# Performance work log

Measured on AMD Instinct MI355X. Metric: run time of the kernel, lower is better.

The kernel has to match this reference:

```python
import jax, jax.numpy as jnp
import numpy as np
from jax import lax

EPS = 1e-5
GROUPS = 16

def _conv(x, w, b):
    # x: [N,C,H,W], w: [O,I,3,3]
    y = lax.conv_general_dilated(x, w, (1, 1), 'SAME',
                                 dimension_numbers=('NCHW', 'OIHW', 'NCHW'))
    return y + b[None, :, None, None]

def _group_norm(x, gamma, beta):
    N, C, H, W = x.shape
    xr = x.reshape(N, GROUPS, C // GROUPS, H, W)
    m = xr.mean(axis=(2, 3, 4), keepdims=True)
    v = xr.var(axis=(2, 3, 4), keepdims=True)
    xn = ((xr - m) * lax.rsqrt(v + EPS)).reshape(N, C, H, W)
    return xn * gamma[None, :, None, None] + beta[None, :, None, None]

def _tower(x, ws, bs, gs, betas):
    for w, b, g, bt in zip(ws, bs, gs, betas):
        x = jax.nn.relu(_group_norm(_conv(x, w, b), g, bt))
    return x

def _fcos_heads(feats, cls_w, cls_b, cls_g, cls_bt, cls_ow, cls_ob,
                reg_w, reg_b, reg_g, reg_bt, reg_ow, reg_ob, ctr_w, ctr_b):
    outs = []
    for f in feats:
        N = f.shape[0]
        c = _tower(f, cls_w, cls_b, cls_g, cls_bt)
        logits = _conv(c, cls_ow, cls_ob)                 # [N, num_classes, H, W]
        r = _tower(f, reg_w, reg_b, reg_g, reg_bt)
        bbox = jax.nn.relu(_conv(r, reg_ow, reg_ob))      # [N, 4, H, W]
        ctr = _conv(r, ctr_w, ctr_b)                      # [N, 1, H, W]
        lvl = jnp.concatenate([logits, bbox, ctr], axis=1)  # [N, num_classes+5, H, W]
        outs.append(lvl.reshape(N, lvl.shape[1], -1))
    return jnp.concatenate(outs, axis=-1)  # [N, num_classes+5, sum(H*W)]

def setup_inputs() -> dict:
    key = jax.random.key(0)
    C, NUM_CLASSES, NB = 256, 80, 2
    sizes = [(128, 128), (64, 64), (32, 32), (16, 16), (8, 8)]
    keys = iter(jax.random.split(key, 64))
    d = {}
    for i, (h, w) in enumerate(sizes):
        d[f'feat{i}'] = jax.random.normal(next(keys), (NB, C, h, w), jnp.float32)
    for head in ('cls', 'reg'):
        for i in range(3):
            d[f'{head}_w{i}'] = 0.01 * jax.random.normal(next(keys), (C, C, 3, 3), jnp.float32)
            d[f'{head}_b{i}'] = jnp.zeros((C,), jnp.float32)
            d[f'{head}_gn_g{i}'] = jnp.ones((C,), jnp.float32)
            d[f'{head}_gn_b{i}'] = jnp.zeros((C,), jnp.float32)
    d['cls_out_w'] = 0.01 * jax.random.normal(next(keys), (NUM_CLASSES, C, 3, 3), jnp.float32)
    prior = 0.01
    d['cls_out_b'] = jnp.full((NUM_CLASSES,), float(-np.log((1 - prior) / prior)), jnp.float32)
    d['reg_out_w'] = 0.01 * jax.random.normal(next(keys), (4, C, 3, 3), jnp.float32)
    d['reg_out_b'] = jnp.zeros((4,), jnp.float32)
    d['ctr_w'] = 0.01 * jax.random.normal(next(keys), (1, C, 3, 3), jnp.float32)
    d['ctr_b'] = jnp.zeros((1,), jnp.float32)
    return d

def reference(feat0, feat1, feat2, feat3, feat4,
              cls_w0, cls_b0, cls_gn_g0, cls_gn_b0,
              cls_w1, cls_b1, cls_gn_g1, cls_gn_b1,
              cls_w2, cls_b2, cls_gn_g2, cls_gn_b2,
              reg_w0, reg_b0, reg_gn_g0, reg_gn_b0,
              reg_w1, reg_b1, reg_gn_g1, reg_gn_b1,
              reg_w2, reg_b2, reg_gn_g2, reg_gn_b2,
              cls_out_w, cls_out_b, reg_out_w, reg_out_b, ctr_w, ctr_b):
    feats = [feat0, feat1, feat2, feat3, feat4]
    return _fcos_heads(feats,
                       [cls_w0, cls_w1, cls_w2], [cls_b0, cls_b1, cls_b2],
                       [cls_gn_g0, cls_gn_g1, cls_gn_g2], [cls_gn_b0, cls_gn_b1, cls_gn_b2],
                       cls_out_w, cls_out_b,
                       [reg_w0, reg_w1, reg_w2], [reg_b0, reg_b1, reg_b2],
                       [reg_gn_g0, reg_gn_g1, reg_gn_g2], [reg_gn_b0, reg_gn_b1, reg_gn_b2],
                       reg_out_w, reg_out_b, ctr_w, ctr_b)
```

## Files before the change

kernel.cpp:

```cpp
#include <hip/hip_runtime.h>
#include <stdint.h>


typedef __attribute__((ext_vector_type(8))) short short8;
typedef __attribute__((ext_vector_type(4))) float floatx4;

#define XP 349184
#define TIB (32 * XP)

__device__ __forceinline__ unsigned short f2bf(float f) {
  unsigned u = __float_as_uint(f);
  u = (u + 0x7FFFu + ((u >> 16) & 1u)) >> 16;
  return (unsigned short)u;
}
__device__ __forceinline__ unsigned pk2(float a, float b) {
  return (unsigned)f2bf(a) | ((unsigned)f2bf(b) << 16);
}
__device__ __forceinline__ void async16(const void* g, void* l) {
  __builtin_amdgcn_global_load_lds(
      (const __attribute__((address_space(1))) unsigned int*)g,
      (__attribute__((address_space(3))) unsigned int*)l, 16, 0, 0);
}

#define WAIT_VM4 0x0F74
#define WAIT_VM0 0x0F70

__device__ const int d_lw[5]   = {7, 6, 5, 4, 3};
__device__ const int d_off[5]  = {0, 16384, 20480, 21504, 21760};
__device__ const int d_nt[5]   = {128, 32, 8, 2, 1};
__device__ const int d_cumT[6] = {0, 1024, 1280, 1344, 1360, 1368};
__device__ const int d_cumO[6] = {0, 512, 640, 672, 680, 684};
__device__ const int d_cumS[6] = {0, 256, 320, 336, 340, 341};
__device__ const int ck_lvl[13] = {0,0,0,0,0,0,0,0,1,1,2,3,4};
__device__ const int ck_c0[13]  = {0,2048,4096,6144,8192,10240,12288,14336,0,2048,0,0,0};
__device__ const int ck_len[13] = {2048,2048,2048,2048,2048,2048,2048,2048,2048,2048,1024,256,64};

__global__ void zpk(float* zp, float* stats) {
  for (int i = threadIdx.x; i < 384; i += 256) zp[i] = 0.f;
  for (int i = threadIdx.x; i < 1920; i += 256) stats[i] = 0.f;
}

__global__ __launch_bounds__(256) void wtrans(
    const float* __restrict__ c0, const float* __restrict__ c1, const float* __restrict__ c2,
    const float* __restrict__ r0, const float* __restrict__ r1, const float* __restrict__ r2,
    const float* __restrict__ cw, const float* __restrict__ rw, const float* __restrict__ tw,
    unsigned short* __restrict__ dst) {
  const int z = blockIdx.y;
  const int nel = (z < 6) ? 589824 : 294912;
  const int idx = blockIdx.x * 256 + threadIdx.x;
  if (idx >= nel) return;
  int tmp = idx;
  const int j = tmp & 7;   tmp >>= 3;
  const int m = tmp & 127; tmp >>= 7;
  const int cs = tmp & 3;  tmp >>= 2;
  const int t = tmp % 9;   tmp /= 9;
  const int cc = tmp & 7;  const int mt = tmp >> 3;
  const int o = mt * 128 + m;
  const int i = cc * 32 + cs * 8 + j;
  float v = 0.f;
  const float* srcs[6] = {c0, c1, c2, r0, r1, r2};
  if (z < 6)      v = srcs[z][((size_t)o * 256 + i) * 9 + t];
  else if (z == 6){ if (o < 80) v = cw[((size_t)o * 256 + i) * 9 + t]; }
  else            { if (o < 4)  v = rw[((size_t)o * 256 + i) * 9 + t];
                    else if (o == 4) v = tw[(size_t)i * 9 + t]; }
  const size_t base = (z < 6) ? (size_t)z * 589824
                              : (size_t)6 * 589824 + (size_t)(z - 6) * 294912;
  dst[base + idx] = f2bf(v);
}

__global__ __launch_bounds__(256) void feat_nhwc(
    const float* __restrict__ s0, const float* __restrict__ s1,
    const float* __restrict__ s2, const float* __restrict__ s3,
    const float* __restrict__ s4, unsigned short* __restrict__ dst) {
  __shared__ unsigned short tile[64][65];
  int bx = blockIdx.x, lvl = 0;
  while (bx >= d_cumS[lvl + 1]) ++lvl;
  const int HW = 1 << (2 * d_lw[lvl]), off = d_off[lvl];
  const float* srcs[5] = {s0, s1, s2, s3, s4};
  const float* src = srcs[lvl];
  const int img = blockIdx.z, c0 = blockIdx.y * 64, p0 = (bx - d_cumS[lvl]) * 64;
  const float* s = src + ((size_t)img * 256 + c0) * HW + p0;
  const int tid = threadIdx.x;
#pragma unroll
  for (int i = 0; i < 4; i++) {
    const int cl = (tid >> 4) + i * 16, pl = (tid & 15) * 4;
    const float4 v = *(const float4*)(s + (size_t)cl * HW + pl);
    tile[cl][pl]     = f2bf(v.x);
    tile[cl][pl + 1] = f2bf(v.y);
    tile[cl][pl + 2] = f2bf(v.z);
    tile[cl][pl + 3] = f2bf(v.w);
  }
  __syncthreads();
  const int pl = tid >> 2, cseg = (tid & 3) * 16;
  unsigned ro[8];
#pragma unroll
  for (int k = 0; k < 8; k++)
    ro[k] = (unsigned)tile[cseg + 2 * k][pl] | ((unsigned)tile[cseg + 2 * k + 1][pl] << 16);
  const int ch0 = c0 + cseg;
  char* db = (char*)dst + (size_t)img * TIB + (size_t)(ch0 >> 3) * XP
           + (size_t)(off + p0 + pl) * 16;
  uint4 u0 = {ro[0], ro[1], ro[2], ro[3]};
  uint4 u1 = {ro[4], ro[5], ro[6], ro[7]};
  *(uint4*)db = u0;
  *(uint4*)(db + XP) = u1;
}

__global__ __launch_bounds__(256) void conv_mfma(
    const unsigned short* __restrict__ xin0, const unsigned short* __restrict__ xin1,
    const unsigned short* __restrict__ wA, const unsigned short* __restrict__ wB,
    unsigned short* __restrict__ y0, unsigned short* __restrict__ y1,
    const float* __restrict__ cb0, const float* __restrict__ cb1,
    float* __restrict__ out,
    const float* __restrict__ ob_cls, const float* __restrict__ ob_reg, const float* __restrict__ ob_ctr,
    const unsigned short* __restrict__ zp, int mode) {
  __shared__ __align__(16) char smem[49152];
  const int tid = threadIdx.x;
  const int* cum = (mode == 0) ? d_cumT : d_cumO;
  const int nwg = (mode == 0) ? 1368 : 684;
  const int xcd = blockIdx.x & 7, cidx = blockIdx.x >> 3;
  const int qq = nwg >> 3, rr = nwg & 7;
  int bid = (xcd < rr ? xcd * (qq + 1) : rr * (qq + 1) + (xcd - rr) * qq) + cidx;
  int lvl = 0;
  while (bid >= cum[lvl + 1]) ++lvl;
  int r = bid - cum[lvl];
  const int lw = d_lw[lvl], W = 1 << lw, HW = 1 << (2 * lw), poffl = d_off[lvl];
  const int ntc = d_nt[lvl];
  const int nt = r % ntc; r /= ntc;
  int mt = 0;
  if (mode == 0) { mt = r & 1; r >>= 1; }
  const int img = r & 1, tower = r >> 1;

  const unsigned short* xin = (tower ? xin1 : xin0) + (size_t)img * 21824 * 256;
  const unsigned short* wset = tower ? wB : wA;

  const int n = tid & 127;
  const int p = nt * 128 + n;
  const bool pv = p < HW;
  const int h = p >> lw, w = p & (W - 1);
  const int kq = tid >> 7;

  const char* xb = (const char*)xin;
  const char* tb[9];
  int stp[9];
#pragma unroll
  for (int t = 0; t < 9; t++) {
    const int rr2 = h + t / 3 - 1, cx = w + t % 3 - 1;
    const bool v = pv && rr2 >= 0 && rr2 < W && cx >= 0 && cx < W;
    tb[t] = v ? xb + (size_t)kq * XP + (size_t)(poffl + rr2 * W + cx) * 16
              : (const char*)zp;
    stp[t] = v ? 4 * XP : 0;
  }

  const char* abase = (const char*)wset + (size_t)mt * 589824;
  const char* a_tid = abase + (size_t)tid * 16;
  char* l_tid = smem + tid * 16;

  const int lane = tid & 63, q = lane >> 4, lr = lane & 15;
  const int wv = tid >> 6, wm = wv >> 1, wn = wv & 1;
  int aoff[4], boff[4];
#pragma unroll
  for (int i = 0; i < 4; i++) {
    aoff[i] = ((q << 7) + wm * 64 + i * 16 + lr) << 4;
    boff[i] = (((q << 7) + wn * 64 + i * 16 + lr) << 4) + 8192;
  }

  floatx4 acc[4][4];
#pragma unroll
  for (int i = 0; i < 4; i++)
#pragma unroll
    for (int j = 0; j < 4; j++) acc[i][j] = (floatx4){0.f, 0.f, 0.f, 0.f};

#define UNIT(CC, U, WIMM)                                                     \
  {                                                                           \
    const int it_ = (CC) * 9 + (U);                                           \
    __builtin_amdgcn_s_waitcnt(WIMM);                                         \
    __builtin_amdgcn_s_barrier();                                             \
    asm volatile("" ::: "memory");                                            \
    if (it_ + 2 < 72) {                                                       \
      const int nu_ = (U) + 2;                                                \
      const int tn_ = nu_ % 9;                              \
      const int ccn_ = (CC) + nu_ / 9;                                        \
      char* la_ = l_tid + (nu_ % 3) * 16384;                                  \
      const char* ap_ = a_tid + (size_t)(it_ + 2) * 8192;                     \
      async16(ap_, la_);                                                      \
      async16(ap_ + 4096, la_ + 4096);                                        \
      const int sp_ = stp[tn_];                                               \
      const char* bp_ = tb[tn_] + ccn_ * sp_;                                 \
      async16(bp_, la_ + 8192);                                               \
      async16(bp_ + (sp_ >> 1), la_ + 12288);                                 \
    }                                                                         \
    asm volatile("" ::: "memory");                                            \
    const int sb_ = ((U) % 3) * 16384;                                        \
    short8 af[4], bfr[4];                                                     \
    _Pragma("unroll")                                                         \
    for (int i = 0; i < 4; i++) {                                             \
      af[i] = *(const short8*)(smem + sb_ + aoff[i]);                         \
      bfr[i] = *(const short8*)(smem + sb_ + boff[i]);                        \
    }                                                                         \
    _Pragma("unroll")                                                         \
    for (int i = 0; i < 4; i++)                                               \
      _Pragma("unroll")                                                       \
      for (int j = 0; j < 4; j++)                                             \
        acc[i][j] = __builtin_amdgcn_mfma_f32_16x16x32_bf16(af[i], bfr[j],    \
                                                            acc[i][j], 0, 0, 0); \
  }

  async16(a_tid, l_tid);
  async16(a_tid + 4096, l_tid + 4096);
  async16(tb[0], l_tid + 8192);
  async16(tb[0] + (stp[0] >> 1), l_tid + 12288);
  async16(a_tid + 8192, l_tid + 16384);
  async16(a_tid + 12288, l_tid + 20480);
  async16(tb[1], l_tid + 24576);
  async16(tb[1] + (stp[1] >> 1), l_tid + 28672);

  for (int cc = 0; cc < 7; ++cc) {
#pragma unroll
    for (int u = 0; u < 9; ++u) UNIT(cc, u, WAIT_VM4)
  }
  UNIT(7, 0, WAIT_VM4) UNIT(7, 1, WAIT_VM4) UNIT(7, 2, WAIT_VM4)
  UNIT(7, 3, WAIT_VM4) UNIT(7, 4, WAIT_VM4) UNIT(7, 5, WAIT_VM4)
  UNIT(7, 6, WAIT_VM4) UNIT(7, 7, WAIT_VM0) UNIT(7, 8, WAIT_VM0)
#undef UNIT

  if (mode == 0) {
    char* yb = (char*)(tower ? y1 : y0) + (size_t)img * TIB;
    const float* cb = tower ? cb1 : cb0;
#pragma unroll
    for (int i = 0; i < 4; i++) {
      const int c = mt * 128 + wm * 64 + i * 16 + (q << 2);
      const float4 b4 = *(const float4*)(cb + c);
      char* yp = yb + (size_t)(c >> 3) * XP + (size_t)poffl * 16 + ((c & 7) << 1);
#pragma unroll
      for (int j = 0; j < 4; j++) {
        const int pp = nt * 128 + wn * 64 + j * 16 + lr;
        if (pp >= HW) continue;
        floatx4 a = acc[i][j];
        uint2 u;
        u.x = pk2(a.x + b4.x, a.y + b4.y);
        u.y = pk2(a.z + b4.z, a.w + b4.w);
        *(uint2*)(yp + (size_t)pp * 16) = u;
      }
    }
  } else {
#pragma unroll
    for (int j = 0; j < 4; j++) {
      const int pp = nt * 128 + wn * 64 + j * 16 + lr;
      if (pp >= HW) continue;
      const size_t gp = (size_t)poffl + pp;
#pragma unroll
      for (int i = 0; i < 4; i++) {
        const int m0 = wm * 64 + i * 16 + (q << 2);
        floatx4 a = acc[i][j];
#pragma unroll
        for (int k2 = 0; k2 < 4; k2++) {
          const int m = m0 + k2;
          const float v = a[k2];
          if (tower == 0) {
            if (m < 80) out[((size_t)img * 85 + m) * 21824 + gp] = v + ob_cls[m];
          } else {
            if (m < 4)
              out[((size_t)img * 85 + 80 + m) * 21824 + gp] = fmaxf(v + ob_reg[m], 0.f);
            else if (m == 4)
              out[((size_t)img * 85 + 84) * 21824 + gp] = v + ob_ctr[0];
          }
        }
      }
    }
  }
}

__global__ __launch_bounds__(256) void gn_stats(
    const unsigned short* __restrict__ y0, const unsigned short* __restrict__ y1,
    float* __restrict__ stats) {
  const int ck = blockIdx.x, g = blockIdx.y, tz = blockIdx.z;
  const int tower = tz >> 1, img = tz & 1;
  const int lvl = ck_lvl[ck], c0 = ck_c0[ck], len = ck_len[ck];
  const char* base = (const char*)(tower ? y1 : y0) + (size_t)img * TIB
                   + (size_t)(2 * g) * XP + (size_t)(d_off[lvl] + c0) * 16;
  const int tid = threadIdx.x;
  float s = 0.f, s2 = 0.f;
  const int n2 = 2 * len;
  for (int i = tid; i < n2; i += 256) {
    const int pl = (i >= len);
    const int pos = i - pl * len;
    const uint4 d = *(const uint4*)(base + (size_t)pl * XP + (size_t)pos * 16);
    unsigned uu[4] = {d.x, d.y, d.z, d.w};
#pragma unroll
    for (int k = 0; k < 4; k++) {
      const float f0 = __uint_as_float(uu[k] << 16);
      const float f1 = __uint_as_float(uu[k] & 0xFFFF0000u);
      s += f0 + f1;
      s2 += f0 * f0 + f1 * f1;
    }
  }
#pragma unroll
  for (int m = 1; m < 64; m <<= 1) {
    s += __shfl_xor(s, m);
    s2 += __shfl_xor(s2, m);
  }
  __shared__ float rs[4], rq[4];
  const int lane = tid & 63, wvv = tid >> 6;
  if (lane == 0) { rs[wvv] = s; rq[wvv] = s2; }
  __syncthreads();
  if (tid == 0) {
    float* st = stats + (((tz * 5 + lvl) * 16 + g) << 1);
    atomicAdd(st, rs[0] + rs[1] + rs[2] + rs[3]);
    atomicAdd(st + 1, rq[0] + rq[1] + rq[2] + rq[3]);
  }
}

__global__ __launch_bounds__(256) void gn_apply(
    const unsigned short* __restrict__ ybase, unsigned short* __restrict__ xbase,
    const float* __restrict__ stats,
    const float* __restrict__ g0, const float* __restrict__ b0,
    const float* __restrict__ g1, const float* __restrict__ b1) {
  const int g = blockIdx.x * 256 + threadIdx.x;
  const int pos = g % 21824;
  const int rest = g / 21824;
  const int plane = rest & 31;
  const int ti = rest >> 5;
  const int tower = ti >> 1;
  const int lvl = (pos >= 16384) + (pos >= 20480) + (pos >= 21504) + (pos >= 21760);
  const float cnt = (float)(16 << (2 * d_lw[lvl]));
  const float* st = stats + ((((ti * 5 + lvl) * 16 + (plane >> 1))) << 1);
  const float mean = st[0] / cnt;
  const float var = st[1] / cnt - mean * mean;
  const float rstd = rsqrtf(var + 1e-5f);
  const float* gam = (tower ? g1 : g0) + plane * 8;
  const float* bet = (tower ? b1 : b0) + plane * 8;
  const size_t off = (size_t)ti * TIB + (size_t)plane * XP + (size_t)pos * 16;
  const uint4 d = *(const uint4*)((const char*)ybase + off);
  unsigned uu[4] = {d.x, d.y, d.z, d.w};
  unsigned ro[4];
#pragma unroll
  for (int k = 0; k < 4; k++) {
    const float f0 = __uint_as_float(uu[k] << 16);
    const float f1 = __uint_as_float(uu[k] & 0xFFFF0000u);
    const float o0 = fmaxf((f0 - mean) * rstd * gam[2 * k] + bet[2 * k], 0.f);
    const float o1 = fmaxf((f1 - mean) * rstd * gam[2 * k + 1] + bet[2 * k + 1], 0.f);
    ro[k] = (unsigned)f2bf(o0) | ((unsigned)f2bf(o1) << 16);
  }
  uint4 od = {ro[0], ro[1], ro[2], ro[3]};
  *(uint4*)((char*)xbase + off) = od;
}

extern "C" void kernel_launch(void* const* d_in, const int* in_sizes, int n_in,
                              void* d_out, int out_size, void* d_ws, size_t ws_size,
                              hipStream_t stream) {
  (void)in_sizes; (void)n_in; (void)out_size; (void)ws_size;
  char* ws = (char*)d_ws;
  unsigned short* zp = (unsigned short*)ws;
  unsigned short* wblk = (unsigned short*)(ws + 2048);
  const size_t WSET_T = 1179648;
  const size_t WSET_O = 589824;
  char* pXfeat = ws + 2048 + 6 * WSET_T + 2 * WSET_O;
  const size_t XSZ = (size_t)2 * 21824 * 256 * 2;
  char* pX = pXfeat + XSZ;
  char* pY = pX + 2 * XSZ;
  float* stats = (float*)(pY + 2 * XSZ);

  zpk<<<1, 256, 0, stream>>>((float*)zp, stats);
  wtrans<<<dim3(2304, 8), 256, 0, stream>>>(
      (const float*)d_in[5], (const float*)d_in[9], (const float*)d_in[13],
      (const float*)d_in[17], (const float*)d_in[21], (const float*)d_in[25],
      (const float*)d_in[29], (const float*)d_in[31], (const float*)d_in[33], wblk);
  feat_nhwc<<<dim3(341, 4, 2), 256, 0, stream>>>(
      (const float*)d_in[0], (const float*)d_in[1], (const float*)d_in[2],
      (const float*)d_in[3], (const float*)d_in[4], (unsigned short*)pXfeat);

  unsigned short* xc = (unsigned short*)pX;
  unsigned short* xr = (unsigned short*)(pX + XSZ);
  unsigned short* yc = (unsigned short*)pY;
  unsigned short* yr = (unsigned short*)(pY + XSZ);

  for (int s = 0; s < 3; s++) {
    const unsigned short* in0 = s ? xc : (unsigned short*)pXfeat;
    const unsigned short* in1 = s ? xr : (unsigned short*)pXfeat;
    const unsigned short* wc = wblk + (size_t)s * 589824;
    const unsigned short* wr = wblk + (size_t)(3 + s) * 589824;
    float* st_s = stats + (size_t)s * 640;
    conv_mfma<<<1368, 256, 0, stream>>>(
        in0, in1, wc, wr, yc, yr,
        (const float*)d_in[6 + 4 * s], (const float*)d_in[18 + 4 * s],
        nullptr, nullptr, nullptr, nullptr, zp, 0);
    gn_stats<<<dim3(13, 16, 4), 256, 0, stream>>>(yc, yr, st_s);
    gn_apply<<<10912, 256, 0, stream>>>(
        (const unsigned short*)pY, (unsigned short*)pX, st_s,
        (const float*)d_in[7 + 4 * s], (const float*)d_in[8 + 4 * s],
        (const float*)d_in[19 + 4 * s], (const float*)d_in[20 + 4 * s]);
  }
  const unsigned short* wo_c = wblk + (size_t)6 * 589824;
  const unsigned short* wo_r = wo_c + 294912;
  conv_mfma<<<684, 256, 0, stream>>>(
      xc, xr, wo_c, wo_r, nullptr, nullptr, nullptr, nullptr,
      (float*)d_out, (const float*)d_in[30], (const float*)d_in[32],
      (const float*)d_in[34], zp, 1);
}
```

Before: 600.6 us.

## Add 128x256 tile conv kernel with triple-buffered async LDS pipeline for tower convs

Adds a new tower-conv kernel in which each block computes a 128-channel by 256-pixel tile, with every wave accumulating 4x8 MFMA fragments. Operands stream through a three-stage async global-to-LDS ring buffer, prefetching two steps ahead. Blocks are remapped across XCDs and the grid drops from 1368 to 688 blocks. The larger tile cuts redundant weight and activation loads per output, at the cost of 72KB LDS per block, heavy register use, fewer blocks, and wasted work on the small pyramid levels.

```diff
diff --git a/kernel.cpp b/kernel.cpp
--- a/kernel.cpp
+++ b/kernel.cpp
@@ -23,6 +23,7 @@
 }
 
 #define WAIT_VM4 0x0F74
+#define WAIT_VM6 0x0F76
 #define WAIT_VM0 0x0F70
 
 __device__ const int d_lw[5]   = {7, 6, 5, 4, 3};
@@ -31,6 +32,8 @@
 __device__ const int d_cumT[6] = {0, 1024, 1280, 1344, 1360, 1368};
 __device__ const int d_cumO[6] = {0, 512, 640, 672, 680, 684};
 __device__ const int d_cumS[6] = {0, 256, 320, 336, 340, 341};
+__device__ const int d_nt2[5]  = {64, 16, 4, 1, 1};
+__device__ const int d_cum2[6] = {0, 512, 640, 672, 680, 688};
 __device__ const int ck_lvl[13] = {0,0,0,0,0,0,0,0,1,1,2,3,4};
 __device__ const int ck_c0[13]  = {0,2048,4096,6144,8192,10240,12288,14336,0,2048,0,0,0};
 __device__ const int ck_len[13] = {2048,2048,2048,2048,2048,2048,2048,2048,2048,2048,1024,256,64};
@@ -270,6 +273,140 @@
   }
 }
 
+__global__ __launch_bounds__(256, 2) void conv_t256(
+    const unsigned short* __restrict__ xin0, const unsigned short* __restrict__ xin1,
+    const unsigned short* __restrict__ wA, const unsigned short* __restrict__ wB,
+    unsigned short* __restrict__ y0, unsigned short* __restrict__ y1,
+    const float* __restrict__ cb0, const float* __restrict__ cb1,
+    const unsigned short* __restrict__ zp) {
+  extern __shared__ __align__(16) char smem[];
+  const int tid = threadIdx.x;
+  const int xcd = blockIdx.x & 7, cidx = blockIdx.x >> 3;
+  int bid = xcd * 86 + cidx;
+  int lvl = 0;
+  while (bid >= d_cum2[lvl + 1]) ++lvl;
+  int r = bid - d_cum2[lvl];
+  const int lw = d_lw[lvl], W = 1 << lw, HW = 1 << (2 * lw), poffl = d_off[lvl];
+  const int ntc = d_nt2[lvl];
+  const int nt = r % ntc; r /= ntc;
+  const int mt = r & 1; r >>= 1;
+  const int img = r & 1, tower = r >> 1;
+
+  const char* xb = (const char*)((tower ? xin1 : xin0)) + (size_t)img * TIB;
+  const unsigned short* wset = tower ? wB : wA;
+
+  const int p = nt * 256 + tid;
+  const bool pv = p < HW;
+  const int h = p >> lw, w = p & (W - 1);
+
+  const char* tb[9];
+  int stp[9];
+#pragma unroll
+  for (int t = 0; t < 9; t++) {
+    const int rr2 = h + t / 3 - 1, cx = w + t % 3 - 1;
+    const bool v = pv && rr2 >= 0 && rr2 < W && cx >= 0 && cx < W;
+    tb[t] = v ? xb + (size_t)(poffl + rr2 * W + cx) * 16 : (const char*)zp;
+    stp[t] = v ? XP : 0;
+  }
+
+  const char* abase = (const char*)wset + (size_t)mt * 589824;
+  const char* a_tid = abase + (size_t)tid * 16;
+  char* l_tid = smem + tid * 16;
+
+  const int lane = tid & 63, q = lane >> 4, lr = lane & 15;
+  const int wv = tid >> 6, wm = wv >> 1, wn = wv & 1;
+  int aoff[4], boff[8];
+#pragma unroll
+  for (int i = 0; i < 4; i++)
+    aoff[i] = ((q << 7) + wm * 64 + i * 16 + lr) << 4;
+#pragma unroll
+  for (int j = 0; j < 8; j++)
+    boff[j] = 8192 + (((q << 8) + wn * 128 + j * 16 + lr) << 4);
+
+  floatx4 acc[4][8];
+#pragma unroll
+  for (int i = 0; i < 4; i++)
+#pragma unroll
+    for (int j = 0; j < 8; j++) acc[i][j] = (floatx4){0.f, 0.f, 0.f, 0.f};
+
+#define TUNIT(CC, U, WIMM)                                                    \
+  {                                                                           \
+    const int it_ = (CC) * 9 + (U);                                           \
+    __builtin_amdgcn_s_waitcnt(WIMM);                                         \
+    __builtin_amdgcn_s_barrier();                                             \
+    asm volatile("" ::: "memory");                                            \
+    if (it_ + 2 < 72) {                                                       \
+      const int nu_ = (U) + 2;                                                \
+      const int tn_ = nu_ % 9;                              \
+      const int ccn_ = (CC) + nu_ / 9;                                        \
+      char* la_ = l_tid + (nu_ % 3) * 24576;                                  \
+      const char* ap_ = a_tid + (size_t)(it_ + 2) * 8192;                     \
+      async16(ap_, la_);                                                      \
+      async16(ap_ + 4096, la_ + 4096);                                        \
+      const int sp_ = stp[tn_];                                               \
+      const char* bp_ = tb[tn_] + ccn_ * 4 * sp_;                             \
+      async16(bp_, la_ + 8192);                                               \
+      async16(bp_ + sp_, la_ + 12288);                                        \
+      async16(bp_ + 2 * sp_, la_ + 16384);                                    \
+      async16(bp_ + 3 * sp_, la_ + 20480);                                    \
+    }                                                                         \
+    asm volatile("" ::: "memory");                                            \
+    const int sb_ = ((U) % 3) * 24576;                                        \
+    short8 af[4], bfr[8];                                                     \
+    _Pragma("unroll")                                                         \
+    for (int i = 0; i < 4; i++) af[i] = *(const short8*)(smem + sb_ + aoff[i]); \
+    _Pragma("unroll")                                                         \
+    for (int j = 0; j < 8; j++) bfr[j] = *(const short8*)(smem + sb_ + boff[j]); \
+    _Pragma("unroll")                                                         \
+    for (int i = 0; i < 4; i++)                                               \
+      _Pragma("unroll")                                                       \
+      for (int j = 0; j < 8; j++)                                             \
+        acc[i][j] = __builtin_amdgcn_mfma_f32_16x16x32_bf16(af[i], bfr[j],    \
+                                                            acc[i][j], 0, 0, 0); \
+  }
+
+  async16(a_tid, l_tid);
+  async16(a_tid + 4096, l_tid + 4096);
+  async16(tb[0], l_tid + 8192);
+  async16(tb[0] + stp[0], l_tid + 12288);
+  async16(tb[0] + 2 * stp[0], l_tid + 16384);
+  async16(tb[0] + 3 * stp[0], l_tid + 20480);
+  async16(a_tid + 8192, l_tid + 24576);
+  async16(a_tid + 12288, l_tid + 28672);
+  async16(tb[1], l_tid + 32768);
+  async16(tb[1] + stp[1], l_tid + 36864);
+  async16(tb[1] + 2 * stp[1], l_tid + 40960);
+  async16(tb[1] + 3 * stp[1], l_tid + 45056);
+
+  for (int cc = 0; cc < 7; ++cc) {
+#pragma unroll
+    for (int u = 0; u < 9; ++u) TUNIT(cc, u, WAIT_VM6)
+  }
+  TUNIT(7, 0, WAIT_VM6) TUNIT(7, 1, WAIT_VM6) TUNIT(7, 2, WAIT_VM6)
+  TUNIT(7, 3, WAIT_VM6) TUNIT(7, 4, WAIT_VM6) TUNIT(7, 5, WAIT_VM6)
+  TUNIT(7, 6, WAIT_VM6) TUNIT(7, 7, WAIT_VM0) TUNIT(7, 8, WAIT_VM0)
+#undef TUNIT
+
+  char* yb = (char*)(tower ? y1 : y0) + (size_t)img * TIB;
+  const float* cb = tower ? cb1 : cb0;
+#pragma unroll
+  for (int i = 0; i < 4; i++) {
+    const int c = mt * 128 + wm * 64 + i * 16 + (q << 2);
+    const float4 b4 = *(const float4*)(cb + c);
+    char* yp = yb + (size_t)(c >> 3) * XP + (size_t)poffl * 16 + ((c & 7) << 1);
+#pragma unroll
+    for (int j = 0; j < 8; j++) {
+      const int pp = nt * 256 + wn * 128 + j * 16 + lr;
+      if (pp >= HW) continue;
+      floatx4 a = acc[i][j];
+      uint2 u;
+      u.x = pk2(a.x + b4.x, a.y + b4.y);
+      u.y = pk2(a.z + b4.z, a.w + b4.w);
+      *(uint2*)(yp + (size_t)pp * 16) = u;
+    }
+  }
+}
+
 __global__ __launch_bounds__(256) void gn_stats(
     const unsigned short* __restrict__ y0, const unsigned short* __restrict__ y1,
     float* __restrict__ stats) {
@@ -360,6 +497,9 @@
   char* pY = pX + 2 * XSZ;
   float* stats = (float*)(pY + 2 * XSZ);
 
+  hipFuncSetAttribute(reinterpret_cast<const void*>(conv_t256),
+                      hipFuncAttributeMaxDynamicSharedMemorySize, 73728);
+
   zpk<<<1, 256, 0, stream>>>((float*)zp, stats);
   wtrans<<<dim3(2304, 8), 256, 0, stream>>>(
       (const float*)d_in[5], (const float*)d_in[9], (const float*)d_in[13],
@@ -380,10 +520,9 @@
     const unsigned short* wc = wblk + (size_t)s * 589824;
     const unsigned short* wr = wblk + (size_t)(3 + s) * 589824;
     float* st_s = stats + (size_t)s * 640;
-    conv_mfma<<<1368, 256, 0, stream>>>(
+    conv_t256<<<688, 256, 73728, stream>>>(
         in0, in1, wc, wr, yc, yr,
-        (const float*)d_in[6 + 4 * s], (const float*)d_in[18 + 4 * s],
-        nullptr, nullptr, nullptr, nullptr, zp, 0);
+        (const float*)d_in[6 + 4 * s], (const float*)d_in[18 + 4 * s], zp);
     gn_stats<<<dim3(13, 16, 4), 256, 0, stream>>>(yc, yr, st_s);
     gn_apply<<<10912, 256, 0, stream>>>(
         (const unsigned short*)pY, (unsigned short*)pX, st_s,
```

Result: slower. 641.9 us (+6.9%).
